# Optimization experiments

Measured on AMD Instinct MI355X. Metric: run time of the kernel, lower is better.

## Reference

```python
import jax, jax.numpy as jnp
import numpy as np
import math

B, S, D = 8, 2048, 512
H, DH = 8, 64  # heads, head dim

def setup_inputs() -> dict:
    key = jax.random.key(0)
    ks = jax.random.split(key, 13)
    w = 0.02
    return {
        "x_Q": jax.random.normal(ks[0], (B, S, D), jnp.float32),
        "x_K": jax.random.normal(ks[1], (B, S, D), jnp.float32),
        "x_V": jax.random.normal(ks[2], (B, S, D), jnp.float32),
        "Wq": jax.random.normal(ks[3], (H * DH, D), jnp.float32) * w,
        "bq": jnp.zeros((H * DH,), jnp.float32),
        "Wk": jax.random.normal(ks[4], (H * DH, D), jnp.float32) * w,
        "bk": jnp.zeros((H * DH,), jnp.float32),
        "Wv": jax.random.normal(ks[5], (H * DH, D), jnp.float32) * w,
        "bv": jnp.zeros((H * DH,), jnp.float32),
        "Wo": jax.random.normal(ks[6], (D, H * DH), jnp.float32) * w,
        "bo": jnp.zeros((D,), jnp.float32),
        "src_batch_lens": jax.random.randint(ks[7], (B,), 1, S + 1, jnp.int32),
    }

def reference(x_Q, x_K, x_V, Wq, bq, Wk, bk, Wv, bv, Wo, bo, src_batch_lens):
    b, s, _ = x_Q.shape
    # projections (torch Linear: x @ W.T + b), split into heads
    Q = (x_Q @ Wq.T + bq).reshape(b, s, H, DH)
    K = (x_K @ Wk.T + bk).reshape(b, s, H, DH)
    V = (x_V @ Wv.T + bv).reshape(b, s, H, DH)
    scale = 1.0 / math.sqrt(DH)
    # [b, h, q, k] scores
    scores = jnp.einsum('bqhd,bkhd->bhqk', Q * scale, K)
    # padding mask on key positions >= src_batch_lens[i], filled with -1e9
    key_mask = jnp.arange(s)[None, :] >= src_batch_lens[:, None]  # [b, k]
    scores = jnp.where(key_mask[:, None, None, :], -1.0e9, scores)
    attn = jax.nn.softmax(scores, axis=-1)  # dropout p=0.0 -> identity
    ctx = jnp.einsum('bhqk,bkhd->bqhd', attn, V).reshape(b, s, H * DH)
    return ctx @ Wo.T + bo
```

## Files before the change

kernel.cpp:

```cpp
#include <hip/hip_runtime.h>
#include <math.h>

#define NB 8
#define NS 2048
#define ND 512
#define NHH 8
#define NDH 64

typedef __attribute__((ext_vector_type(4))) float f32x4;
typedef __attribute__((ext_vector_type(8))) short bf16x8;
typedef unsigned short ush;

__device__ inline ush f2bf_rne(float f) {
    unsigned u = __float_as_uint(f);
    unsigned r = u + 0x7FFFu + ((u >> 16) & 1u);
    return (ush)(r >> 16);
}
__device__ inline float bf2f(ush h) { return __uint_as_float(((unsigned)h) << 16); }

__device__ inline unsigned cvt_pk_bf16(float lo, float hi) {
    unsigned r;
    asm("v_cvt_pk_bf16_f32 %0, %1, %2" : "=v"(r) : "v"(lo), "v"(hi));
    return r;
}

#if defined(__has_builtin)
#if __has_builtin(__builtin_amdgcn_exp2f)
#define EXP2F(x) __builtin_amdgcn_exp2f(x)
#else
#define EXP2F(x) exp2f(x)
#endif
#else
#define EXP2F(x) exp2f(x)
#endif

#define GLL16(gp, lp) __builtin_amdgcn_global_load_lds( \
    (const __attribute__((address_space(1))) unsigned int*)(gp), \
    (__attribute__((address_space(3))) unsigned int*)(lp), 16, 0, 0)

__global__ __launch_bounds__(256) void conv_w_kernel(
    const float* __restrict__ Wq, const float* __restrict__ Wk,
    const float* __restrict__ Wv, const float* __restrict__ Wo,
    ush* __restrict__ wbf, ush* __restrict__ wo_hi, ush* __restrict__ wo_lo)
{
    const int y = blockIdx.y;
    const int i = (blockIdx.x * 256 + threadIdx.x) * 4;
    if (y < 3) {
        const float* src = (y == 0) ? Wq : (y == 1) ? Wk : Wv;
        const float4 v = *(const float4*)&src[i];
        ushort4 o;
        o.x = f2bf_rne(v.x); o.y = f2bf_rne(v.y);
        o.z = f2bf_rne(v.z); o.w = f2bf_rne(v.w);
        *(ushort4*)&wbf[y * 262144 + i] = o;
    } else {
        const float4 v = *(const float4*)&Wo[i];
        ushort4 hi, lo;
        hi.x = f2bf_rne(v.x); lo.x = f2bf_rne(v.x - bf2f(hi.x));
        hi.y = f2bf_rne(v.y); lo.y = f2bf_rne(v.y - bf2f(hi.y));
        hi.z = f2bf_rne(v.z); lo.z = f2bf_rne(v.z - bf2f(hi.z));
        hi.w = f2bf_rne(v.w); lo.w = f2bf_rne(v.w - bf2f(hi.w));
        *(ushort4*)&wo_hi[i] = hi;
        *(ushort4*)&wo_lo[i] = lo;
    }
}

__global__ __launch_bounds__(256) void qkv_gemm_kernel(
    const float* __restrict__ xq, const float* __restrict__ xk, const float* __restrict__ xv,
    const ush* __restrict__ wbf,
    const float* __restrict__ bq, const float* __restrict__ bk, const float* __restrict__ bv,
    ush* __restrict__ Qb, ush* __restrict__ Kb, ush* __restrict__ VT)
{
    __shared__ ush As[2][4096];
    __shared__ ush Bs[2][4096];

    const int z = blockIdx.z;
    const float* X    = (z == 0) ? xq : (z == 1) ? xk : xv;
    const ush*   W    = wbf + z * 262144;
    const float* bias = (z == 0) ? bq : (z == 1) ? bk : bv;

    const int t = threadIdx.x;
    const int w = t >> 6, l = t & 63;
    const int l15 = l & 15, g = l >> 4;
    const int m0 = blockIdx.x * 128, n0 = blockIdx.y * 128;
    const int wm = (w & 1) << 6, wn = (w >> 1) << 6;

    const int srow = l >> 2;
    const int sg   = (l & 3) ^ ((srow + (srow >> 2)) & 3);
    const int fsw  = (g ^ ((l15 + (l15 >> 2)) & 3)) << 3;
    const int c0   = w * 2;

    f32x4 acc[4][4];
    #pragma unroll
    for (int i = 0; i < 4; ++i)
        #pragma unroll
        for (int j = 0; j < 4; ++j) acc[i][j] = (f32x4)(0.0f);

    {
        const size_t ar0 = (size_t)(m0 + c0 * 16 + srow) * 512 + sg * 8;
        const size_t ar1 = (size_t)(m0 + (c0 + 1) * 16 + srow) * 512 + sg * 8;
        const float4 a0 = *(const float4*)&X[ar0];
        const float4 a1 = *(const float4*)&X[ar0 + 4];
        const float4 a2 = *(const float4*)&X[ar1];
        const float4 a3 = *(const float4*)&X[ar1 + 4];
        GLL16(&W[(size_t)(n0 + c0 * 16 + srow) * 512 + sg * 8], &Bs[0][c0 * 512 + l * 8]);
        GLL16(&W[(size_t)(n0 + (c0 + 1) * 16 + srow) * 512 + sg * 8], &Bs[0][(c0 + 1) * 512 + l * 8]);
        uint4 u0, u1;
        u0.x = (unsigned)f2bf_rne(a0.x) | ((unsigned)f2bf_rne(a0.y) << 16);
        u0.y = (unsigned)f2bf_rne(a0.z) | ((unsigned)f2bf_rne(a0.w) << 16);
        u0.z = (unsigned)f2bf_rne(a1.x) | ((unsigned)f2bf_rne(a1.y) << 16);
        u0.w = (unsigned)f2bf_rne(a1.z) | ((unsigned)f2bf_rne(a1.w) << 16);
        u1.x = (unsigned)f2bf_rne(a2.x) | ((unsigned)f2bf_rne(a2.y) << 16);
        u1.y = (unsigned)f2bf_rne(a2.z) | ((unsigned)f2bf_rne(a2.w) << 16);
        u1.z = (unsigned)f2bf_rne(a3.x) | ((unsigned)f2bf_rne(a3.y) << 16);
        u1.w = (unsigned)f2bf_rne(a3.z) | ((unsigned)f2bf_rne(a3.w) << 16);
        *(uint4*)&As[0][c0 * 512 + l * 8] = u0;
        *(uint4*)&As[0][(c0 + 1) * 512 + l * 8] = u1;
        __syncthreads();
    }

    for (int ki = 0; ki < 16; ++ki) {
        const int buf = ki & 1;
        const int ktn = (ki + 1) * 32;
        float4 a0, a1, a2, a3;
        if (ki < 15) {
            const size_t ar0 = (size_t)(m0 + c0 * 16 + srow) * 512 + ktn + sg * 8;
            const size_t ar1 = (size_t)(m0 + (c0 + 1) * 16 + srow) * 512 + ktn + sg * 8;
            a0 = *(const float4*)&X[ar0];
            a1 = *(const float4*)&X[ar0 + 4];
            a2 = *(const float4*)&X[ar1];
            a3 = *(const float4*)&X[ar1 + 4];
            GLL16(&W[(size_t)(n0 + c0 * 16 + srow) * 512 + ktn + sg * 8], &Bs[buf ^ 1][c0 * 512 + l * 8]);
            GLL16(&W[(size_t)(n0 + (c0 + 1) * 16 + srow) * 512 + ktn + sg * 8], &Bs[buf ^ 1][(c0 + 1) * 512 + l * 8]);
        }

        bf16x8 af[4], bfr[4];
        #pragma unroll
        for (int mi = 0; mi < 4; ++mi)
            af[mi] = *(const bf16x8*)&As[buf][(((w & 1) << 2) + mi) * 512 + l15 * 32 + fsw];
        #pragma unroll
        for (int ni = 0; ni < 4; ++ni)
            bfr[ni] = *(const bf16x8*)&Bs[buf][(((w >> 1) << 2) + ni) * 512 + l15 * 32 + fsw];
        #pragma unroll
        for (int mi = 0; mi < 4; ++mi)
            #pragma unroll
            for (int ni = 0; ni < 4; ++ni)
                acc[mi][ni] = __builtin_amdgcn_mfma_f32_16x16x32_bf16(af[mi], bfr[ni], acc[mi][ni], 0, 0, 0);

        if (ki < 15) {
            uint4 u0, u1;
            u0.x = (unsigned)f2bf_rne(a0.x) | ((unsigned)f2bf_rne(a0.y) << 16);
            u0.y = (unsigned)f2bf_rne(a0.z) | ((unsigned)f2bf_rne(a0.w) << 16);
            u0.z = (unsigned)f2bf_rne(a1.x) | ((unsigned)f2bf_rne(a1.y) << 16);
            u0.w = (unsigned)f2bf_rne(a1.z) | ((unsigned)f2bf_rne(a1.w) << 16);
            u1.x = (unsigned)f2bf_rne(a2.x) | ((unsigned)f2bf_rne(a2.y) << 16);
            u1.y = (unsigned)f2bf_rne(a2.z) | ((unsigned)f2bf_rne(a2.w) << 16);
            u1.z = (unsigned)f2bf_rne(a3.x) | ((unsigned)f2bf_rne(a3.y) << 16);
            u1.w = (unsigned)f2bf_rne(a3.z) | ((unsigned)f2bf_rne(a3.w) << 16);
            *(uint4*)&As[buf ^ 1][c0 * 512 + l * 8] = u0;
            *(uint4*)&As[buf ^ 1][(c0 + 1) * 512 + l * 8] = u1;
        }
        __syncthreads();
    }

    const float qscale = (z == 0) ? 0.18033688011112042f : 1.0f;
    float bnv[4];
    #pragma unroll
    for (int ni = 0; ni < 4; ++ni) bnv[ni] = bias[n0 + wn + ni * 16 + l15];

    if (z < 2) {
        ush* O = (z == 0) ? Qb : Kb;
        #pragma unroll
        for (int mi = 0; mi < 4; ++mi) {
            #pragma unroll
            for (int ni = 0; ni < 4; ++ni) {
                const int n = n0 + wn + ni * 16 + l15;
                const int hh = n >> 6, dh = n & 63;
                #pragma unroll
                for (int r = 0; r < 4; ++r) {
                    const int m = m0 + wm + mi * 16 + (g << 2) + r;
                    const int bi = m >> 11, s = m & (NS - 1);
                    O[((size_t)(bi * 8 + hh) * 2048 + s) * 64 + dh] =
                        f2bf_rne((acc[mi][ni][r] + bnv[ni]) * qscale);
                }
            }
        }
    } else {
        #pragma unroll
        for (int mi = 0; mi < 4; ++mi) {
            #pragma unroll
            for (int ni = 0; ni < 4; ++ni) {
                const int n = n0 + wn + ni * 16 + l15;
                const int hh = n >> 6, dh = n & 63;
                const int mb = m0 + wm + mi * 16 + (g << 2);
                const int bi = mb >> 11, s = mb & (NS - 1);
                ushort4 pk;
                pk.x = f2bf_rne(acc[mi][ni][0] + bnv[ni]);
                pk.y = f2bf_rne(acc[mi][ni][1] + bnv[ni]);
                pk.z = f2bf_rne(acc[mi][ni][2] + bnv[ni]);
                pk.w = f2bf_rne(acc[mi][ni][3] + bnv[ni]);
                *(ushort4*)&VT[((size_t)(bi * 8 + hh) * 64 + dh) * 2048 + s] = pk;
            }
        }
    }
}

__global__ __launch_bounds__(256) void attn_kernel(
    ush* __restrict__ Qb, const ush* __restrict__ Kb,
    const ush* __restrict__ VT, const int* __restrict__ lens,
    ush* __restrict__ ctx_lo)
{
    __shared__ ush Ps[128 * 72];
    __shared__ ush Vt[2 * 4624];

    const int tid = threadIdx.x;
    const int w = tid >> 6, l = tid & 63;
    const int l15 = l & 15, g = l >> 4;

    const int id = blockIdx.x;
    const int h = id & 7, qt = (id >> 3) & 15, b = id >> 7;
    const int L = lens[b];
    const int q0 = qt << 7;
    const size_t bh = ((size_t)b * 8 + h) * 2048;

    const ush* qptr = Qb + (bh + q0 + w * 16 + l15) * 64 + g * 8;
    const bf16x8 qfa0 = *(const bf16x8*)(qptr);
    const bf16x8 qfa1 = *(const bf16x8*)(qptr + 32);
    const bf16x8 qfb0 = *(const bf16x8*)(qptr + 64 * 64);
    const bf16x8 qfb1 = *(const bf16x8*)(qptr + 64 * 64 + 32);

    const ush* kbase = Kb + (bh + l15) * 64 + g * 8;

    const int dv = tid >> 2, seg = (tid & 3) << 4;
    const ush* vbase = VT + bh * 64 + (size_t)dv * 2048 + seg;
    const int vt_off = dv * 72 + ((dv >> 4) << 3) + seg;

    ush* psw_a = &Ps[(w * 16 + l15) * 72 + (g << 2)];
    const ush* pp_a = &Ps[(w * 16 + l15) * 72 + g * 8];
    ush* psw_b = psw_a + 64 * 72;
    const ush* pp_b = pp_a + 64 * 72;

    bf16x8 ones;
    #pragma unroll
    for (int j = 0; j < 8; ++j) ones[j] = (short)0x3F80;

    f32x4 oa[4], ob[4];
    f32x4 ola = (f32x4)(0.0f), olb = (f32x4)(0.0f);
    #pragma unroll
    for (int i = 0; i < 4; ++i) { oa[i] = (f32x4)(0.0f); ob[i] = (f32x4)(0.0f); }

    f32x4 spa[4], spb[4];
    const int T = (L + 63) >> 6;

    {
        const uint4 v0 = *(const uint4*)(vbase);
        const uint4 v1 = *(const uint4*)(vbase + 8);
        #pragma unroll
        for (int st = 0; st < 4; ++st) { spa[st] = (f32x4)(0.0f); spb[st] = (f32x4)(0.0f); }
        __builtin_amdgcn_s_setprio(1);
        #pragma unroll
        for (int st = 0; st < 4; ++st) {
            const bf16x8 kf0 = *(const bf16x8*)(kbase + st * 1024);
            const bf16x8 kf1 = *(const bf16x8*)(kbase + st * 1024 + 32);
            spa[st] = __builtin_amdgcn_mfma_f32_16x16x32_bf16(kf0, qfa0, spa[st], 0, 0, 0);
            spa[st] = __builtin_amdgcn_mfma_f32_16x16x32_bf16(kf1, qfa1, spa[st], 0, 0, 0);
            spb[st] = __builtin_amdgcn_mfma_f32_16x16x32_bf16(kf0, qfb0, spb[st], 0, 0, 0);
            spb[st] = __builtin_amdgcn_mfma_f32_16x16x32_bf16(kf1, qfb1, spb[st], 0, 0, 0);
        }
        __builtin_amdgcn_s_setprio(0);
        ush* dst = &Vt[vt_off];
        *(uint4*)dst = v0;
        *(uint4*)(dst + 8) = v1;
        __syncthreads();
    }

    auto finish = [&](const ush* vb, bool masked, int kb0) {
        uint2 pka[4], pkb[4];
        #pragma unroll
        for (int st = 0; st < 4; ++st) {
            float pa[4], pb[4];
            #pragma unroll
            for (int r = 0; r < 4; ++r) {
                float ea = EXP2F(spa[st][r]);
                float eb = EXP2F(spb[st][r]);
                if (masked) {
                    const int key = kb0 + st * 16 + (g << 2) + r;
                    ea = (key < L) ? ea : 0.0f;
                    eb = (key < L) ? eb : 0.0f;
                }
                pa[r] = ea; pb[r] = eb;
            }
            pka[st].x = cvt_pk_bf16(pa[0], pa[1]);
            pka[st].y = cvt_pk_bf16(pa[2], pa[3]);
            pkb[st].x = cvt_pk_bf16(pb[0], pb[1]);
            pkb[st].y = cvt_pk_bf16(pb[2], pb[3]);
        }
        #pragma unroll
        for (int st = 0; st < 4; ++st) {
            *(uint2*)(psw_a + st * 16) = pka[st];
            *(uint2*)(psw_b + st * 16) = pkb[st];
        }
        const bf16x8 pfa0 = *(const bf16x8*)(pp_a);
        const bf16x8 pfa1 = *(const bf16x8*)(pp_a + 32);
        const bf16x8 pfb0 = *(const bf16x8*)(pp_b);
        const bf16x8 pfb1 = *(const bf16x8*)(pp_b + 32);
        __builtin_amdgcn_s_setprio(1);
        ola = __builtin_amdgcn_mfma_f32_16x16x32_bf16(pfa0, ones, ola, 0, 0, 0);
        ola = __builtin_amdgcn_mfma_f32_16x16x32_bf16(pfa1, ones, ola, 0, 0, 0);
        olb = __builtin_amdgcn_mfma_f32_16x16x32_bf16(pfb0, ones, olb, 0, 0, 0);
        olb = __builtin_amdgcn_mfma_f32_16x16x32_bf16(pfb1, ones, olb, 0, 0, 0);
        #pragma unroll
        for (int st2 = 0; st2 < 4; ++st2) {
            const ush* vp = vb + (st2 * 16 + l15) * 72 + (st2 << 3) + g * 8;
            const bf16x8 vf0 = *(const bf16x8*)(vp);
            const bf16x8 vf1 = *(const bf16x8*)(vp + 32);
            oa[st2] = __builtin_amdgcn_mfma_f32_16x16x32_bf16(pfa0, vf0, oa[st2], 0, 0, 0);
            oa[st2] = __builtin_amdgcn_mfma_f32_16x16x32_bf16(pfa1, vf1, oa[st2], 0, 0, 0);
            ob[st2] = __builtin_amdgcn_mfma_f32_16x16x32_bf16(pfb0, vf0, ob[st2], 0, 0, 0);
            ob[st2] = __builtin_amdgcn_mfma_f32_16x16x32_bf16(pfb1, vf1, ob[st2], 0, 0, 0);
        }
        __builtin_amdgcn_s_setprio(0);
    };

    for (int t = 1; t < T; ++t) {
        const int k0 = t << 6;
        bf16x8 kf[8];
        const ush* kp = kbase + (size_t)k0 * 64;
        #pragma unroll
        for (int st = 0; st < 4; ++st) {
            kf[2 * st]     = *(const bf16x8*)(kp + st * 1024);
            kf[2 * st + 1] = *(const bf16x8*)(kp + st * 1024 + 32);
        }
        const uint4 nv0 = *(const uint4*)(vbase + k0);
        const uint4 nv1 = *(const uint4*)(vbase + k0 + 8);

        finish(&Vt[((t & 1) ^ 1) * 4624], false, 0);

        #pragma unroll
        for (int st = 0; st < 4; ++st) { spa[st] = (f32x4)(0.0f); spb[st] = (f32x4)(0.0f); }
        __builtin_amdgcn_s_setprio(1);
        #pragma unroll
        for (int st = 0; st < 4; ++st) {
            spa[st] = __builtin_amdgcn_mfma_f32_16x16x32_bf16(kf[2 * st], qfa0, spa[st], 0, 0, 0);
            spa[st] = __builtin_amdgcn_mfma_f32_16x16x32_bf16(kf[2 * st + 1], qfa1, spa[st], 0, 0, 0);
            spb[st] = __builtin_amdgcn_mfma_f32_16x16x32_bf16(kf[2 * st], qfb0, spb[st], 0, 0, 0);
            spb[st] = __builtin_amdgcn_mfma_f32_16x16x32_bf16(kf[2 * st + 1], qfb1, spb[st], 0, 0, 0);
        }
        __builtin_amdgcn_s_setprio(0);

        ush* dst = &Vt[(t & 1) * 4624 + vt_off];
        *(uint4*)dst = nv0;
        *(uint4*)(dst + 8) = nv1;
        __syncthreads();
    }

    finish(&Vt[((T - 1) & 1) * 4624], true, (T - 1) << 6);

    #pragma unroll
    for (int r = 0; r < 4; ++r) {
        const float inva = 1.0f / ola[r];
        const float invb = 1.0f / olb[r];
        const size_t rowa = bh + q0 + w * 16 + (g << 2) + r;
        const size_t rowb = rowa + 64;
        #pragma unroll
        for (int st2 = 0; st2 < 4; ++st2) {
            const float va = oa[st2][r] * inva;
            const ush ha = f2bf_rne(va);
            Qb[rowa * 64 + st2 * 16 + l15] = ha;
            ctx_lo[rowa * 64 + st2 * 16 + l15] = f2bf_rne(va - bf2f(ha));
            const float vbv = ob[st2][r] * invb;
            const ush hb = f2bf_rne(vbv);
            Qb[rowb * 64 + st2 * 16 + l15] = hb;
            ctx_lo[rowb * 64 + st2 * 16 + l15] = f2bf_rne(vbv - bf2f(hb));
        }
    }
}

__global__ __launch_bounds__(256) void out_gemm_kernel(
    const ush* __restrict__ ctx_hi, const ush* __restrict__ ctx_lo,
    const ush* __restrict__ wo_hi, const ush* __restrict__ wo_lo,
    const float* __restrict__ bo, float* __restrict__ out)
{
    __shared__ ush Ah[2][4096], Al[2][4096], Bh[2][4096], Bl[2][4096];

    const int t = threadIdx.x;
    const int w = t >> 6, l = t & 63;
    const int l15 = l & 15, g = l >> 4;
    const int m0 = blockIdx.x * 128, n0 = blockIdx.y * 128;
    const int wm = (w & 1) << 6, wn = (w >> 1) << 6;

    const int srow = l >> 2;
    const int sg   = (l & 3) ^ ((srow + (srow >> 2)) & 3);
    const int fsw  = (g ^ ((l15 + (l15 >> 2)) & 3)) << 3;
    const int c0   = w * 2;

    f32x4 acc[4][4];
    #pragma unroll
    for (int i = 0; i < 4; ++i)
        #pragma unroll
        for (int j = 0; j < 4; ++j) acc[i][j] = (f32x4)(0.0f);

    auto stage = [&](int bf, int kt) {
        #pragma unroll
        for (int cc = 0; cc < 2; ++cc) {
            const int c = c0 + cc;
            const int m = m0 + c * 16 + srow;
            const int k = kt + sg * 8;
            const size_t ga = ((size_t)((m >> 11) * 8 + (k >> 6)) * 2048 + (m & (NS - 1))) * 64 + (k & 63);
            GLL16(&ctx_hi[ga], &Ah[bf][c * 512 + l * 8]);
            GLL16(&ctx_lo[ga], &Al[bf][c * 512 + l * 8]);
            const size_t gb = (size_t)(n0 + c * 16 + srow) * 512 + kt + sg * 8;
            GLL16(&wo_hi[gb], &Bh[bf][c * 512 + l * 8]);
            GLL16(&wo_lo[gb], &Bl[bf][c * 512 + l * 8]);
        }
    };

    stage(0, 0);
    __syncthreads();

    for (int ki = 0; ki < 16; ++ki) {
        const int buf = ki & 1;
        if (ki < 15) stage(buf ^ 1, (ki + 1) * 32);

        bf16x8 ah[4], al[4], bh4[4], bl4[4];
        #pragma unroll
        for (int mi = 0; mi < 4; ++mi) {
            const int off = (((w & 1) << 2) + mi) * 512 + l15 * 32 + fsw;
            ah[mi] = *(const bf16x8*)&Ah[buf][off];
            al[mi] = *(const bf16x8*)&Al[buf][off];
        }
        #pragma unroll
        for (int ni = 0; ni < 4; ++ni) {
            const int off = (((w >> 1) << 2) + ni) * 512 + l15 * 32 + fsw;
            bh4[ni] = *(const bf16x8*)&Bh[buf][off];
            bl4[ni] = *(const bf16x8*)&Bl[buf][off];
        }
        #pragma unroll
        for (int mi = 0; mi < 4; ++mi)
            #pragma unroll
            for (int ni = 0; ni < 4; ++ni) {
                acc[mi][ni] = __builtin_amdgcn_mfma_f32_16x16x32_bf16(ah[mi], bh4[ni], acc[mi][ni], 0, 0, 0);
                acc[mi][ni] = __builtin_amdgcn_mfma_f32_16x16x32_bf16(al[mi], bh4[ni], acc[mi][ni], 0, 0, 0);
                acc[mi][ni] = __builtin_amdgcn_mfma_f32_16x16x32_bf16(ah[mi], bl4[ni], acc[mi][ni], 0, 0, 0);
            }
        __syncthreads();
    }

    float bov[4];
    #pragma unroll
    for (int ni = 0; ni < 4; ++ni) bov[ni] = bo[n0 + wn + ni * 16 + l15];

    #pragma unroll
    for (int mi = 0; mi < 4; ++mi)
        #pragma unroll
        for (int ni = 0; ni < 4; ++ni) {
            const int n = n0 + wn + ni * 16 + l15;
            #pragma unroll
            for (int r = 0; r < 4; ++r) {
                const int m = m0 + wm + mi * 16 + (g << 2) + r;
                out[(size_t)m * 512 + n] = acc[mi][ni][r] + bov[ni];
            }
        }
}

extern "C" void kernel_launch(void* const* d_in, const int* in_sizes, int n_in,
                              void* d_out, int out_size, void* d_ws, size_t ws_size,
                              hipStream_t stream)
{
    const float* xq   = (const float*)d_in[0];
    const float* xk   = (const float*)d_in[1];
    const float* xv   = (const float*)d_in[2];
    const float* Wq   = (const float*)d_in[3];
    const float* bq   = (const float*)d_in[4];
    const float* Wk   = (const float*)d_in[5];
    const float* bk   = (const float*)d_in[6];
    const float* Wv   = (const float*)d_in[7];
    const float* bv   = (const float*)d_in[8];
    const float* Wo   = (const float*)d_in[9];
    const float* bo   = (const float*)d_in[10];
    const int*   lens = (const int*)d_in[11];
    float* out = (float*)d_out;

    const size_t elems = (size_t)NB * NHH * NS * NDH;
    ush* Qb     = (ush*)d_ws;
    ush* Kb     = Qb + elems;
    ush* VT     = Kb + elems;
    ush* ctx_lo = VT + elems;
    ush* wbf    = ctx_lo + elems;
    ush* wo_hi  = wbf + 3 * 262144;
    ush* wo_lo  = wo_hi + 262144;

    const dim3 blk(256);
    conv_w_kernel<<<dim3(256, 4), blk, 0, stream>>>(Wq, Wk, Wv, Wo, wbf, wo_hi, wo_lo);
    qkv_gemm_kernel<<<dim3(128, 4, 3), blk, 0, stream>>>(
        xq, xk, xv, wbf, bq, bk, bv, Qb, Kb, VT);
    attn_kernel<<<dim3(NB * NHH * (NS / 128)), blk, 0, stream>>>(Qb, Kb, VT, lens, ctx_lo);
    out_gemm_kernel<<<dim3(128, 4), blk, 0, stream>>>(Qb, ctx_lo, wo_hi, wo_lo, bo, out);
}
```

Before: 309.8 us.

## Sort attention batches by length, swap grid axes, widen out-GEMM to 512 threads

New measurement: 302.0 us. 1.03x faster.

```diff
diff --git a/kernel.cpp b/kernel.cpp
--- a/kernel.cpp
+++ b/kernel.cpp
@@ -81,7 +81,7 @@
     const int t = threadIdx.x;
     const int w = t >> 6, l = t & 63;
     const int l15 = l & 15, g = l >> 4;
-    const int m0 = blockIdx.x * 128, n0 = blockIdx.y * 128;
+    const int m0 = blockIdx.y * 128, n0 = blockIdx.x * 128;
     const int wm = (w & 1) << 6, wn = (w >> 1) << 6;
 
     const int srow = l >> 2;
@@ -94,6 +94,18 @@
     for (int i = 0; i < 4; ++i)
         #pragma unroll
         for (int j = 0; j < 4; ++j) acc[i][j] = (f32x4)(0.0f);
+
+    auto packA = [&](const float4& a0, const float4& a1, const float4& a2,
+                     const float4& a3, uint4& u0, uint4& u1) {
+        u0.x = cvt_pk_bf16(a0.x, a0.y);
+        u0.y = cvt_pk_bf16(a0.z, a0.w);
+        u0.z = cvt_pk_bf16(a1.x, a1.y);
+        u0.w = cvt_pk_bf16(a1.z, a1.w);
+        u1.x = cvt_pk_bf16(a2.x, a2.y);
+        u1.y = cvt_pk_bf16(a2.z, a2.w);
+        u1.z = cvt_pk_bf16(a3.x, a3.y);
+        u1.w = cvt_pk_bf16(a3.z, a3.w);
+    };
 
     {
         const size_t ar0 = (size_t)(m0 + c0 * 16 + srow) * 512 + sg * 8;
@@ -105,14 +117,7 @@
         GLL16(&W[(size_t)(n0 + c0 * 16 + srow) * 512 + sg * 8], &Bs[0][c0 * 512 + l * 8]);
         GLL16(&W[(size_t)(n0 + (c0 + 1) * 16 + srow) * 512 + sg * 8], &Bs[0][(c0 + 1) * 512 + l * 8]);
         uint4 u0, u1;
-        u0.x = (unsigned)f2bf_rne(a0.x) | ((unsigned)f2bf_rne(a0.y) << 16);
-        u0.y = (unsigned)f2bf_rne(a0.z) | ((unsigned)f2bf_rne(a0.w) << 16);
-        u0.z = (unsigned)f2bf_rne(a1.x) | ((unsigned)f2bf_rne(a1.y) << 16);
-        u0.w = (unsigned)f2bf_rne(a1.z) | ((unsigned)f2bf_rne(a1.w) << 16);
-        u1.x = (unsigned)f2bf_rne(a2.x) | ((unsigned)f2bf_rne(a2.y) << 16);
-        u1.y = (unsigned)f2bf_rne(a2.z) | ((unsigned)f2bf_rne(a2.w) << 16);
-        u1.z = (unsigned)f2bf_rne(a3.x) | ((unsigned)f2bf_rne(a3.y) << 16);
-        u1.w = (unsigned)f2bf_rne(a3.z) | ((unsigned)f2bf_rne(a3.w) << 16);
+        packA(a0, a1, a2, a3, u0, u1);
         *(uint4*)&As[0][c0 * 512 + l * 8] = u0;
         *(uint4*)&As[0][(c0 + 1) * 512 + l * 8] = u1;
         __syncthreads();
@@ -148,14 +153,7 @@
 
         if (ki < 15) {
             uint4 u0, u1;
-            u0.x = (unsigned)f2bf_rne(a0.x) | ((unsigned)f2bf_rne(a0.y) << 16);
-            u0.y = (unsigned)f2bf_rne(a0.z) | ((unsigned)f2bf_rne(a0.w) << 16);
-            u0.z = (unsigned)f2bf_rne(a1.x) | ((unsigned)f2bf_rne(a1.y) << 16);
-            u0.w = (unsigned)f2bf_rne(a1.z) | ((unsigned)f2bf_rne(a1.w) << 16);
-            u1.x = (unsigned)f2bf_rne(a2.x) | ((unsigned)f2bf_rne(a2.y) << 16);
-            u1.y = (unsigned)f2bf_rne(a2.z) | ((unsigned)f2bf_rne(a2.w) << 16);
-            u1.z = (unsigned)f2bf_rne(a3.x) | ((unsigned)f2bf_rne(a3.y) << 16);
-            u1.w = (unsigned)f2bf_rne(a3.z) | ((unsigned)f2bf_rne(a3.w) << 16);
+            packA(a0, a1, a2, a3, u0, u1);
             *(uint4*)&As[buf ^ 1][c0 * 512 + l * 8] = u0;
             *(uint4*)&As[buf ^ 1][(c0 + 1) * 512 + l * 8] = u1;
         }
@@ -169,22 +167,6 @@
 
     if (z < 2) {
         ush* O = (z == 0) ? Qb : Kb;
-        #pragma unroll
-        for (int mi = 0; mi < 4; ++mi) {
-            #pragma unroll
-            for (int ni = 0; ni < 4; ++ni) {
-                const int n = n0 + wn + ni * 16 + l15;
-                const int hh = n >> 6, dh = n & 63;
-                #pragma unroll
-                for (int r = 0; r < 4; ++r) {
-                    const int m = m0 + wm + mi * 16 + (g << 2) + r;
-                    const int bi = m >> 11, s = m & (NS - 1);
-                    O[((size_t)(bi * 8 + hh) * 2048 + s) * 64 + dh] =
-                        f2bf_rne((acc[mi][ni][r] + bnv[ni]) * qscale);
-                }
-            }
-        }
-    } else {
         #pragma unroll
         for (int mi = 0; mi < 4; ++mi) {
             #pragma unroll
@@ -193,12 +175,30 @@
                 const int hh = n >> 6, dh = n & 63;
                 const int mb = m0 + wm + mi * 16 + (g << 2);
                 const int bi = mb >> 11, s = mb & (NS - 1);
-                ushort4 pk;
-                pk.x = f2bf_rne(acc[mi][ni][0] + bnv[ni]);
-                pk.y = f2bf_rne(acc[mi][ni][1] + bnv[ni]);
-                pk.z = f2bf_rne(acc[mi][ni][2] + bnv[ni]);
-                pk.w = f2bf_rne(acc[mi][ni][3] + bnv[ni]);
-                *(ushort4*)&VT[((size_t)(bi * 8 + hh) * 64 + dh) * 2048 + s] = pk;
+                const size_t base = ((size_t)(bi * 8 + hh) * 2048 + s) * 64 + dh;
+                const unsigned u01 = cvt_pk_bf16((acc[mi][ni][0] + bnv[ni]) * qscale,
+                                                 (acc[mi][ni][1] + bnv[ni]) * qscale);
+                const unsigned u23 = cvt_pk_bf16((acc[mi][ni][2] + bnv[ni]) * qscale,
+                                                 (acc[mi][ni][3] + bnv[ni]) * qscale);
+                O[base]           = (ush)u01;
+                O[base + 64]      = (ush)(u01 >> 16);
+                O[base + 128]     = (ush)u23;
+                O[base + 192]     = (ush)(u23 >> 16);
+            }
+        }
+    } else {
+        #pragma unroll
+        for (int mi = 0; mi < 4; ++mi) {
+            #pragma unroll
+            for (int ni = 0; ni < 4; ++ni) {
+                const int n = n0 + wn + ni * 16 + l15;
+                const int hh = n >> 6, dh = n & 63;
+                const int mb = m0 + wm + mi * 16 + (g << 2);
+                const int bi = mb >> 11, s = mb & (NS - 1);
+                uint2 pk;
+                pk.x = cvt_pk_bf16(acc[mi][ni][0] + bnv[ni], acc[mi][ni][1] + bnv[ni]);
+                pk.y = cvt_pk_bf16(acc[mi][ni][2] + bnv[ni], acc[mi][ni][3] + bnv[ni]);
+                *(uint2*)&VT[((size_t)(bi * 8 + hh) * 64 + dh) * 2048 + s] = pk;
             }
         }
     }
@@ -217,8 +217,22 @@
     const int l15 = l & 15, g = l >> 4;
 
     const int id = blockIdx.x;
-    const int h = id & 7, qt = (id >> 3) & 15, b = id >> 7;
-    const int L = lens[b];
+
+    int Ls[8];
+    #pragma unroll
+    for (int j = 0; j < 8; ++j) Ls[j] = lens[j];
+    const int slot = id >> 7;
+    int b = 0;
+    #pragma unroll
+    for (int bb = 0; bb < 8; ++bb) {
+        int r = 0;
+        #pragma unroll
+        for (int j = 0; j < 8; ++j)
+            r += (Ls[j] > Ls[bb]) || (Ls[j] == Ls[bb] && j < bb);
+        if (r == slot) b = bb;
+    }
+    const int h = id & 7, qt = (id >> 3) & 15;
+    const int L = Ls[b];
     const int q0 = qt << 7;
     const size_t bh = ((size_t)b * 8 + h) * 2048;
 
@@ -375,7 +389,7 @@
     }
 }
 
-__global__ __launch_bounds__(256) void out_gemm_kernel(
+__global__ __launch_bounds__(512) void out_gemm_kernel(
     const ush* __restrict__ ctx_hi, const ush* __restrict__ ctx_lo,
     const ush* __restrict__ wo_hi, const ush* __restrict__ wo_lo,
     const float* __restrict__ bo, float* __restrict__ out)
@@ -385,33 +399,30 @@
     const int t = threadIdx.x;
     const int w = t >> 6, l = t & 63;
     const int l15 = l & 15, g = l >> 4;
-    const int m0 = blockIdx.x * 128, n0 = blockIdx.y * 128;
-    const int wm = (w & 1) << 6, wn = (w >> 1) << 6;
+    const int m0 = blockIdx.y * 128, n0 = blockIdx.x * 128;
+    const int wm = (w & 1) << 6, wn = (w >> 1) << 5;
 
     const int srow = l >> 2;
     const int sg   = (l & 3) ^ ((srow + (srow >> 2)) & 3);
     const int fsw  = (g ^ ((l15 + (l15 >> 2)) & 3)) << 3;
-    const int c0   = w * 2;
-
-    f32x4 acc[4][4];
+    const int c0   = w;
+
+    f32x4 acc[4][2];
     #pragma unroll
     for (int i = 0; i < 4; ++i)
         #pragma unroll
-        for (int j = 0; j < 4; ++j) acc[i][j] = (f32x4)(0.0f);
+        for (int j = 0; j < 2; ++j) acc[i][j] = (f32x4)(0.0f);
 
     auto stage = [&](int bf, int kt) {
-        #pragma unroll
-        for (int cc = 0; cc < 2; ++cc) {
-            const int c = c0 + cc;
-            const int m = m0 + c * 16 + srow;
-            const int k = kt + sg * 8;
-            const size_t ga = ((size_t)((m >> 11) * 8 + (k >> 6)) * 2048 + (m & (NS - 1))) * 64 + (k & 63);
-            GLL16(&ctx_hi[ga], &Ah[bf][c * 512 + l * 8]);
-            GLL16(&ctx_lo[ga], &Al[bf][c * 512 + l * 8]);
-            const size_t gb = (size_t)(n0 + c * 16 + srow) * 512 + kt + sg * 8;
-            GLL16(&wo_hi[gb], &Bh[bf][c * 512 + l * 8]);
-            GLL16(&wo_lo[gb], &Bl[bf][c * 512 + l * 8]);
-        }
+        const int c = c0;
+        const int m = m0 + c * 16 + srow;
+        const int k = kt + sg * 8;
+        const size_t ga = ((size_t)((m >> 11) * 8 + (k >> 6)) * 2048 + (m & (NS - 1))) * 64 + (k & 63);
+        GLL16(&ctx_hi[ga], &Ah[bf][c * 512 + l * 8]);
+        GLL16(&ctx_lo[ga], &Al[bf][c * 512 + l * 8]);
+        const size_t gb = (size_t)(n0 + c * 16 + srow) * 512 + kt + sg * 8;
+        GLL16(&wo_hi[gb], &Bh[bf][c * 512 + l * 8]);
+        GLL16(&wo_lo[gb], &Bl[bf][c * 512 + l * 8]);
     };
 
     stage(0, 0);
@@ -421,7 +432,7 @@
         const int buf = ki & 1;
         if (ki < 15) stage(buf ^ 1, (ki + 1) * 32);
 
-        bf16x8 ah[4], al[4], bh4[4], bl4[4];
+        bf16x8 ah[4], al[4], bh4[2], bl4[2];
         #pragma unroll
         for (int mi = 0; mi < 4; ++mi) {
             const int off = (((w & 1) << 2) + mi) * 512 + l15 * 32 + fsw;
@@ -429,15 +440,15 @@
             al[mi] = *(const bf16x8*)&Al[buf][off];
         }
         #pragma unroll
-        for (int ni = 0; ni < 4; ++ni) {
-            const int off = (((w >> 1) << 2) + ni) * 512 + l15 * 32 + fsw;
+        for (int ni = 0; ni < 2; ++ni) {
+            const int off = (((w >> 1) << 1) + ni) * 512 + l15 * 32 + fsw;
             bh4[ni] = *(const bf16x8*)&Bh[buf][off];
             bl4[ni] = *(const bf16x8*)&Bl[buf][off];
         }
         #pragma unroll
         for (int mi = 0; mi < 4; ++mi)
             #pragma unroll
-            for (int ni = 0; ni < 4; ++ni) {
+            for (int ni = 0; ni < 2; ++ni) {
                 acc[mi][ni] = __builtin_amdgcn_mfma_f32_16x16x32_bf16(ah[mi], bh4[ni], acc[mi][ni], 0, 0, 0);
                 acc[mi][ni] = __builtin_amdgcn_mfma_f32_16x16x32_bf16(al[mi], bh4[ni], acc[mi][ni], 0, 0, 0);
                 acc[mi][ni] = __builtin_amdgcn_mfma_f32_16x16x32_bf16(ah[mi], bl4[ni], acc[mi][ni], 0, 0, 0);
@@ -445,14 +456,14 @@
         __syncthreads();
     }
 
-    float bov[4];
-    #pragma unroll
-    for (int ni = 0; ni < 4; ++ni) bov[ni] = bo[n0 + wn + ni * 16 + l15];
+    float bov[2];
+    #pragma unroll
+    for (int ni = 0; ni < 2; ++ni) bov[ni] = bo[n0 + wn + ni * 16 + l15];
 
     #pragma unroll
     for (int mi = 0; mi < 4; ++mi)
         #pragma unroll
-        for (int ni = 0; ni < 4; ++ni) {
+        for (int ni = 0; ni < 2; ++ni) {
             const int n = n0 + wn + ni * 16 + l15;
             #pragma unroll
             for (int r = 0; r < 4; ++r) {
@@ -491,8 +502,8 @@
 
     const dim3 blk(256);
     conv_w_kernel<<<dim3(256, 4), blk, 0, stream>>>(Wq, Wk, Wv, Wo, wbf, wo_hi, wo_lo);
-    qkv_gemm_kernel<<<dim3(128, 4, 3), blk, 0, stream>>>(
+    qkv_gemm_kernel<<<dim3(4, 128, 3), blk, 0, stream>>>(
         xq, xk, xv, wbf, bq, bk, bv, Qb, Kb, VT);
     attn_kernel<<<dim3(NB * NHH * (NS / 128)), blk, 0, stream>>>(Qb, Kb, VT, lens, ctx_lo);
-    out_gemm_kernel<<<dim3(128, 4), blk, 0, stream>>>(Qb, ctx_lo, wo_hi, wo_lo, bo, out);
-}
+    out_gemm_kernel<<<dim3(4, 128), dim3(512), 0, stream>>>(Qb, ctx_lo, wo_hi, wo_lo, bo, out);
+}
```
